# Performance work log

Measured on AMD Instinct MI355X. Metric: run time of the kernel, lower is better.

Reference implementation:

```python
import jax, jax.numpy as jnp
import numpy as np

N, E, IN_F, EDGE_F, HID, S = 200000, 600000, 28, 4, 128, 20000
NUM_LAYERS = 4
L = NUM_LAYERS - 1
BN_EPS = 1e-5


def setup_inputs() -> dict:
    key = jax.random.key(0)
    ks = jax.random.split(key, 20)
    p = lambda k, shape: (jax.random.normal(k, shape, dtype=jnp.float32) * 0.1)
    return {
        'x': jax.random.normal(ks[0], (N, IN_F), dtype=jnp.float32),
        'edge_index': jax.random.randint(ks[1], (2, E), 0, N),
        'edge_attr': jax.random.normal(ks[2], (E, EDGE_F), dtype=jnp.float32),
        'edge_weight': jax.random.uniform(ks[3], (E,), dtype=jnp.float32),
        'node_mask': (jax.random.uniform(ks[4], (N,)) > 0.5).astype(jnp.float32),
        'subgraphs2nodes': jax.random.randint(ks[5], (N,), 0, S),
        # layer-1 params (in_features -> hidden)
        'be1_W1': p(ks[6], (EDGE_F, IN_F)), 'be1_b1': jnp.zeros((IN_F,), jnp.float32),
        'be1_W2': p(ks[7], (IN_F, IN_F)), 'be1_b2': jnp.zeros((IN_F,), jnp.float32),
        'm1_W1': p(ks[8], (IN_F, HID)), 'm1_b1': jnp.zeros((HID,), jnp.float32),
        'm1_W2': p(ks[9], (HID, HID)), 'm1_b2': jnp.zeros((HID,), jnp.float32),
        'bn1_g': jnp.ones((HID,), jnp.float32), 'bn1_b': jnp.zeros((HID,), jnp.float32),
        'eps1': jnp.zeros((), jnp.float32),
        # layers 2..NUM_LAYERS, stacked (hidden -> hidden)
        'beW1': p(ks[10], (L, EDGE_F, HID)), 'beb1': jnp.zeros((L, HID), jnp.float32),
        'beW2': p(ks[11], (L, HID, HID)), 'beb2': jnp.zeros((L, HID), jnp.float32),
        'mW1': p(ks[12], (L, HID, HID)), 'mb1': jnp.zeros((L, HID), jnp.float32),
        'mW2': p(ks[13], (L, HID, HID)), 'mb2': jnp.zeros((L, HID), jnp.float32),
        'bng': jnp.ones((L, HID), jnp.float32), 'bnb': jnp.zeros((L, HID), jnp.float32),
        'eps': jnp.zeros((L,), jnp.float32),
    }


def _mlp2(h, W1, b1, W2, b2):
    # Linear -> ReLU -> Linear
    return jnp.dot(jax.nn.relu(jnp.dot(h, W1) + b1), W2) + b2


def _gine(x, src, dst, edge_attr, edge_weight, eps,
          beW1, beb1, beW2, beb2, W1, b1, W2, b2, g, beta):
    # bond encoder on edge features
    e = _mlp2(edge_attr, beW1, beb1, beW2, beb2)            # [E, d]
    # message: relu(x_j + e_ij) * w_ij, aggregated at dst via scatter-add
    m = jax.nn.relu(x[src] + e) * edge_weight[:, None]      # [E, d]
    aggr = jax.ops.segment_sum(m, dst, num_segments=N)      # [N, d]
    h = (1.0 + eps) * x + aggr
    # node MLP: Linear,ReLU,Linear,BN(train mode),ReLU
    h = _mlp2(h, W1, b1, W2, b2)
    mu = jnp.mean(h, axis=0)
    var = jnp.mean((h - mu) ** 2, axis=0)
    h = (h - mu) * jax.lax.rsqrt(var + BN_EPS) * g + beta
    return jax.nn.relu(h)


def reference(x, edge_index, edge_attr, edge_weight, node_mask, subgraphs2nodes,
              be1_W1, be1_b1, be1_W2, be1_b2, m1_W1, m1_b1, m1_W2, m1_b2,
              bn1_g, bn1_b, eps1,
              beW1, beb1, beW2, beb2, mW1, mb1, mW2, mb2, bng, bnb, eps):
    src, dst = edge_index[0], edge_index[1]
    h = _gine(x, src, dst, edge_attr, edge_weight, eps1,
              be1_W1, be1_b1, be1_W2, be1_b2,
              m1_W1, m1_b1, m1_W2, m1_b2, bn1_g, bn1_b)
    for i in range(L):
        h_new = _gine(h, src, dst, edge_attr, edge_weight, eps[i],
                      beW1[i], beb1[i], beW2[i], beb2[i],
                      mW1[i], mb1[i], mW2[i], mb2[i], bng[i], bnb[i])
        h = h + h_new  # residual
    # float node_mask branch + global_add_pool over subgraphs2nodes
    h = h * node_mask[:, None]
    return jax.ops.segment_sum(h, subgraphs2nodes, num_segments=S)  # [S, HID]
```

## Files before the change

kernel.cpp:

```cpp
#include <hip/hip_runtime.h>
#include <hip/hip_bf16.h>


#define BNEPS 1e-5f
#define LDA 136
#define SCAN_NB 240

typedef __attribute__((ext_vector_type(8))) short bf16x8;
typedef __attribute__((ext_vector_type(8))) unsigned short u16x8;
typedef __attribute__((ext_vector_type(4))) float f32x4;

__device__ inline short f2bf(float f) {
    __hip_bfloat16 h = __float2bfloat16(f);
    return *reinterpret_cast<short*>(&h);
}
__device__ inline unsigned short f2bfu(float f) {
    __hip_bfloat16 h = __float2bfloat16(f);
    return *reinterpret_cast<unsigned short*>(&h);
}
__device__ inline float bf2f(unsigned short u) {
    union { unsigned int i; float f; } v; v.i = ((unsigned int)u) << 16; return v.f;
}


__global__ __launch_bounds__(256) void k_prep(
    const float* __restrict__ m1W2, const float* __restrict__ beW2,
    const float* __restrict__ mW1, const float* __restrict__ mW2,
    short* __restrict__ out)
{
    __shared__ float tileS[64][65];
    int b = blockIdx.x, mat = b >> 2, t = b & 3;
    const float* Wsrc;
    if (mat == 0) Wsrc = m1W2;
    else {
        int l = (mat - 1) / 3, which = (mat - 1) % 3;
        Wsrc = (which == 0) ? beW2 + (size_t)l * 16384
             : (which == 1) ? mW1 + (size_t)l * 16384
             :                mW2 + (size_t)l * 16384;
    }
    short* dst = out + (size_t)mat * 16384;
    int tr = (t >> 1) * 64, tc = (t & 1) * 64;
    for (int i = threadIdx.x; i < 4096; i += 256) {
        int r = i >> 6, c = i & 63;
        tileS[r][c] = Wsrc[(size_t)(tr + r) * 128 + (tc + c)];
    }
    __syncthreads();
    for (int i = threadIdx.x; i < 4096; i += 256) {
        int kl = i & 63, nl = i >> 6;
        int n = tc + nl, k = tr + kl;
        int fo = (((n >> 4) * 4 + (k >> 5)) * 64 + (((k >> 3) & 3) * 16 + (n & 15))) * 8 + (k & 7);
        dst[fo] = f2bf(tileS[kl][nl]);
    }
}

__global__ __launch_bounds__(256) void k_prep1(
    const float* __restrict__ W1, short* __restrict__ out)
{
    for (int i = threadIdx.x; i < 4096; i += 256) {
        int j = i & 7, sub = (i >> 3) & 63, nt = i >> 9;
        int quad = sub >> 4, l15 = sub & 15;
        int n = nt * 16 + l15, k = quad * 8 + j;
        out[i] = (k < 28) ? f2bf(W1[(size_t)k * 128 + n]) : (short)0;
    }
}

__global__ __launch_bounds__(256) void k_prep28(
    const float* __restrict__ W2, short* __restrict__ out)
{
    for (int i = threadIdx.x; i < 32 * 32; i += 256) {
        int n = i >> 5, k = i & 31;
        out[i] = (n < 28 && k < 28) ? f2bf(W2[(size_t)k * 28 + n]) : (short)0;
    }
}

__global__ __launch_bounds__(256) void k_prepx(
    const float* __restrict__ x, unsigned short* __restrict__ xbf, int N)
{
    int total = N * 32;
    for (int i = blockIdx.x * 256 + threadIdx.x; i < total; i += gridDim.x * 256) {
        int n = i >> 5, c = i & 31;
        xbf[i] = (c < 28) ? f2bfu(x[(size_t)n * 28 + c]) : (unsigned short)0;
    }
}

__global__ __launch_bounds__(256) void k_count(
    const int* __restrict__ ei, int* __restrict__ counts, int E)
{
    for (int e = blockIdx.x * 256 + threadIdx.x; e < E; e += gridDim.x * 256)
        atomicAdd(&counts[ei[E + e]], 1);
}

__global__ __launch_bounds__(256) void k_count2(
    const int* __restrict__ s2n, const float* __restrict__ mask,
    int* __restrict__ counts2, int N)
{
    for (int n = blockIdx.x * 256 + threadIdx.x; n < N; n += gridDim.x * 256)
        if (mask[n] != 0.f) atomicAdd(&counts2[s2n[n]], 1);
}

__global__ __launch_bounds__(256) void k_scanA(
    const int* __restrict__ counts, int* __restrict__ bsum, int N, int seg)
{
    __shared__ int red[256];
    int b = blockIdx.x;
    int lo = b * seg, hi = min(lo + seg, N);
    int s = 0;
    for (int i = lo + threadIdx.x; i < hi; i += 256) s += counts[i];
    red[threadIdx.x] = s;
    __syncthreads();
    for (int d = 128; d > 0; d >>= 1) {
        if (threadIdx.x < d) red[threadIdx.x] += red[threadIdx.x + d];
        __syncthreads();
    }
    if (threadIdx.x == 0) bsum[b] = red[0];
}

__global__ __launch_bounds__(256) void k_scanB(
    int* __restrict__ bsum, int nb, int* __restrict__ offs, int N)
{
    __shared__ int sh[256];
    int v = (threadIdx.x < nb) ? bsum[threadIdx.x] : 0;
    sh[threadIdx.x] = v;
    __syncthreads();
    for (int d = 1; d < 256; d <<= 1) {
        int t = (threadIdx.x >= d) ? sh[threadIdx.x - d] : 0;
        __syncthreads();
        sh[threadIdx.x] += t;
        __syncthreads();
    }
    if (threadIdx.x < nb) bsum[threadIdx.x] = sh[threadIdx.x] - v;
    if (threadIdx.x == 0) offs[N] = sh[255];
}

__global__ __launch_bounds__(256) void k_scanC(
    const int* __restrict__ counts, const int* __restrict__ bsum,
    int* __restrict__ offs, int* __restrict__ cursor, int N, int seg)
{
    __shared__ int sh[256];
    int b = blockIdx.x;
    int lo = b * seg, hi = min(lo + seg, N);
    int base = bsum[b];
    for (int t0 = lo; t0 < hi; t0 += 256) {
        int i = t0 + threadIdx.x;
        int v = (i < hi) ? counts[i] : 0;
        sh[threadIdx.x] = v;
        __syncthreads();
        for (int d = 1; d < 256; d <<= 1) {
            int t = (threadIdx.x >= d) ? sh[threadIdx.x - d] : 0;
            __syncthreads();
            sh[threadIdx.x] += t;
            __syncthreads();
        }
        int excl = base + sh[threadIdx.x] - v;
        if (i < hi) { offs[i] = excl; cursor[i] = excl; }
// ... 247 lines not shown
        m += fmaxf(bf2f(xx) + bf2f(ee), 0.f) * __int_as_float(mt.y);
    GSLOT28(mtA, eA, xA, k0)
    GSLOT28(mtB, eB, xB, k0 + 1)
    GSLOT28(mtC, eC, xC, k0 + 2)
    GSLOT28(mtD, eD, xD, k0 + 3)
    int k = k0;
    while (true) {
        GCONS28(mtA, eA, xA)
        GCONS28(mtB, eB, xB)
        GCONS28(mtC, eC, xC)
        GCONS28(mtD, eD, xD)
        k += 4;
        if (k >= k1) break;
        GSLOT28(mtA, eA, xA, k)
        GSLOT28(mtB, eB, xB, k + 1)
        GSLOT28(mtC, eC, xC, k + 2)
        GSLOT28(mtD, eD, xD, k + 3)
    }
    #undef GSLOT28
    #undef GCONS28
    u28[(size_t)n * 28 + lane] = fmaf(s, x[(size_t)n * 28 + lane], m);
}

__global__ __launch_bounds__(512, 2) void k_mlp(
    const unsigned short* __restrict__ src, const short* __restrict__ W1f,
    const float* __restrict__ b1, const short* __restrict__ W2f,
    const float* __restrict__ b2, unsigned short* __restrict__ dst,
    float* __restrict__ stats, int N)
{
    __shared__ short As[256 * LDA];
    __shared__ short Bs1[16384];
    __shared__ short Bs2[16384];
    __shared__ float sstat[256];
    int tid = threadIdx.x;
    for (int i = tid; i < 2048; i += 512) {
        *(bf16x8*)&Bs1[i * 8] = *(const bf16x8*)&W1f[i * 8];
        *(bf16x8*)&Bs2[i * 8] = *(const bf16x8*)&W2f[i * 8];
    }
    if (tid < 256) sstat[tid] = 0.f;
    int w = tid >> 6, lane = tid & 63;
    int l15 = lane & 15, quad = lane >> 4;
    int rb = w * 32;
    float b1r[8], b2r[8], lsum[8], lsq[8];
    #pragma unroll
    for (int nt = 0; nt < 8; ++nt) {
        b1r[nt] = b1[nt * 16 + l15]; b2r[nt] = b2[nt * 16 + l15];
        lsum[nt] = 0.f; lsq[nt] = 0.f;
    }
    int numTiles = (N + 255) >> 8;
    bf16x8 st[8];
    {
        int tile = blockIdx.x;
        if (tile < numTiles) {
            int base = tile * 256;
            #pragma unroll
            for (int kk = 0; kk < 8; ++kk) {
                int i = tid + kk * 512;
                int rr = base + (i >> 4);
                st[kk] = (rr < N) ? *(const bf16x8*)&src[(size_t)rr * 128 + (i & 15) * 8]
                                  : (bf16x8){0, 0, 0, 0, 0, 0, 0, 0};
            }
        }
    }
    __syncthreads();

    for (int tile = blockIdx.x; tile < numTiles; tile += gridDim.x) {
        int base = tile * 256;
        #pragma unroll
        for (int kk = 0; kk < 8; ++kk) {
            int i = tid + kk * 512;
            *(bf16x8*)&As[(i >> 4) * LDA + (i & 15) * 8] = st[kk];
        }
        int tnext = tile + gridDim.x;
        if (tnext < numTiles) {
            int bn = tnext * 256;
            #pragma unroll
            for (int kk = 0; kk < 8; ++kk) {
                int i = tid + kk * 512;
                int rr = bn + (i >> 4);
                st[kk] = (rr < N) ? *(const bf16x8*)&src[(size_t)rr * 128 + (i & 15) * 8]
                                  : (bf16x8){0, 0, 0, 0, 0, 0, 0, 0};
            }
        }
        __syncthreads();
        f32x4 acc[2][8];
        #pragma unroll
        for (int rg = 0; rg < 2; ++rg)
            #pragma unroll
            for (int nt = 0; nt < 8; ++nt) acc[rg][nt] = (f32x4){0.f, 0.f, 0.f, 0.f};
        #pragma unroll
        for (int kt = 0; kt < 4; ++kt) {
            bf16x8 af0 = *(bf16x8*)&As[(rb + l15) * LDA + kt * 32 + quad * 8];
            bf16x8 af1 = *(bf16x8*)&As[(rb + 16 + l15) * LDA + kt * 32 + quad * 8];
            #pragma unroll
            for (int nt = 0; nt < 8; ++nt) {
                bf16x8 bf = *(const bf16x8*)&Bs1[((nt * 4 + kt) * 64 + lane) * 8];
                acc[0][nt] = __builtin_amdgcn_mfma_f32_16x16x32_bf16(af0, bf, acc[0][nt], 0, 0, 0);
                acc[1][nt] = __builtin_amdgcn_mfma_f32_16x16x32_bf16(af1, bf, acc[1][nt], 0, 0, 0);
            }
        }
        #pragma unroll
        for (int rg = 0; rg < 2; ++rg)
            #pragma unroll
            for (int nt = 0; nt < 8; ++nt)
                #pragma unroll
                for (int r = 0; r < 4; ++r)
                    As[(rb + rg * 16 + quad * 4 + r) * LDA + nt * 16 + l15] =
                        f2bf(fmaxf(acc[rg][nt][r] + b1r[nt], 0.f));
        #pragma unroll
        for (int rg = 0; rg < 2; ++rg)
            #pragma unroll
            for (int nt = 0; nt < 8; ++nt) acc[rg][nt] = (f32x4){0.f, 0.f, 0.f, 0.f};
        #pragma unroll
        for (int kt = 0; kt < 4; ++kt) {
            bf16x8 af0 = *(bf16x8*)&As[(rb + l15) * LDA + kt * 32 + quad * 8];
            bf16x8 af1 = *(bf16x8*)&As[(rb + 16 + l15) * LDA + kt * 32 + quad * 8];
            #pragma unroll
            for (int nt = 0; nt < 8; ++nt) {
                bf16x8 bf = *(const bf16x8*)&Bs2[((nt * 4 + kt) * 64 + lane) * 8];
                acc[0][nt] = __builtin_amdgcn_mfma_f32_16x16x32_bf16(af0, bf, acc[0][nt], 0, 0, 0);
                acc[1][nt] = __builtin_amdgcn_mfma_f32_16x16x32_bf16(af1, bf, acc[1][nt], 0, 0, 0);
            }
        }
        #pragma unroll
        for (int rg = 0; rg < 2; ++rg)
            #pragma unroll
            for (int nt = 0; nt < 8; ++nt) {
                int row0 = base + rb + rg * 16 + quad * 4;
                #pragma unroll
                for (int r = 0; r < 4; ++r) {
                    float z = acc[rg][nt][r] + b2r[nt];
                    if (row0 + r < N) { lsum[nt] += z; lsq[nt] = fmaf(z, z, lsq[nt]); }
                    As[(rb + rg * 16 + quad * 4 + r) * LDA + nt * 16 + l15] = f2bf(z);
                }
            }
        #pragma unroll
        for (int it = 0; it < 8; ++it) {
            int arow = rb + it * 4 + quad;
            int rr = base + arow;
            if (rr < N)
                *(bf16x8*)&dst[(size_t)rr * 128 + l15 * 8] = *(bf16x8*)&As[arow * LDA + l15 * 8];
        }
        __syncthreads();
    }
    #pragma unroll
    for (int nt = 0; nt < 8; ++nt) {
        atomicAdd(&sstat[nt * 16 + l15], lsum[nt]);
        atomicAdd(&sstat[128 + nt * 16 + l15], lsq[nt]);
    }
    __syncthreads();
    if (tid < 256) atomicAdd(&stats[tid], sstat[tid]);
}

__global__ __launch_bounds__(512, 2) void k_mlp1(
    const float* __restrict__ u28, const short* __restrict__ W1f,
    const float* __restrict__ b1, const short* __restrict__ W2f,
    const float* __restrict__ b2, unsigned short* __restrict__ dst,
    float* __restrict__ stats, int N)
{
    __shared__ short A28[256 * 40];
    __shared__ short As[256 * LDA];
    __shared__ short Bs1[4096];
    __shared__ short Bs2[16384];
    __shared__ float sstat[256];
    int tid = threadIdx.x;
    if (tid < 512) {
        int i = tid;
        *(bf16x8*)&Bs1[i * 8] = *(const bf16x8*)&W1f[i * 8];
    }
    for (int i = tid; i < 2048; i += 512)
        *(bf16x8*)&Bs2[i * 8] = *(const bf16x8*)&W2f[i * 8];
    for (int i = tid; i < 1024; i += 512) {
        int row = i >> 2, c = 28 + (i & 3);
        A28[row * 40 + c] = 0;
    }
    if (tid < 256) sstat[tid] = 0.f;
    int w = tid >> 6, lane = tid & 63;
    int l15 = lane & 15, quad = lane >> 4;
    int rb = w * 32;
    float b1r[8], b2r[8], lsum[8], lsq[8];
    #pragma unroll
    for (int nt = 0; nt < 8; ++nt) {
        b1r[nt] = b1[nt * 16 + l15]; b2r[nt] = b2[nt * 16 + l15];
        lsum[nt] = 0.f; lsq[nt] = 0.f;
    }
    int numTiles = (N + 255) >> 8;
    float stf[14];
    {
        int tile = blockIdx.x;
        if (tile < numTiles) {
            int base = tile * 256;
            #pragma unroll
            for (int kk = 0; kk < 14; ++kk) {
                int idx = tid + kk * 512;
                int row = idx / 28, col = idx - row * 28;
                int rr = base + row;
                stf[kk] = (rr < N) ? u28[(size_t)rr * 28 + col] : 0.f;
            }
        }
    }
    __syncthreads();

    for (int tile = blockIdx.x; tile < numTiles; tile += gridDim.x) {
        int base = tile * 256;
        #pragma unroll
        for (int kk = 0; kk < 14; ++kk) {
            int idx = tid + kk * 512;
            int row = idx / 28, col = idx - row * 28;
            A28[row * 40 + col] = f2bf(stf[kk]);
        }
        int tnext = tile + gridDim.x;
        if (tnext < numTiles) {
            int bn = tnext * 256;
            #pragma unroll
            for (int kk = 0; kk < 14; ++kk) {
                int idx = tid + kk * 512;
                int row = idx / 28, col = idx - row * 28;
                int rr = bn + row;
                stf[kk] = (rr < N) ? u28[(size_t)rr * 28 + col] : 0.f;
            }
        }
        __syncthreads();
        f32x4 acc[2][8];
        #pragma unroll
        for (int rg = 0; rg < 2; ++rg)
            #pragma unroll
            for (int nt = 0; nt < 8; ++nt) acc[rg][nt] = (f32x4){0.f, 0.f, 0.f, 0.f};
        {
            bf16x8 af0 = *(bf16x8*)&A28[(rb + l15) * 40 + quad * 8];
            bf16x8 af1 = *(bf16x8*)&A28[(rb + 16 + l15) * 40 + quad * 8];
            #pragma unroll
            for (int nt = 0; nt < 8; ++nt) {
                bf16x8 bf = *(const bf16x8*)&Bs1[(nt * 64 + lane) * 8];
                acc[0][nt] = __builtin_amdgcn_mfma_f32_16x16x32_bf16(af0, bf, acc[0][nt], 0, 0, 0);
                acc[1][nt] = __builtin_amdgcn_mfma_f32_16x16x32_bf16(af1, bf, acc[1][nt], 0, 0, 0);
            }
        }
        #pragma unroll
        for (int rg = 0; rg < 2; ++rg)
            #pragma unroll
            for (int nt = 0; nt < 8; ++nt)
                #pragma unroll
                for (int r = 0; r < 4; ++r)
                    As[(rb + rg * 16 + quad * 4 + r) * LDA + nt * 16 + l15] =
                        f2bf(fmaxf(acc[rg][nt][r] + b1r[nt], 0.f));
        __syncthreads();
        #pragma unroll
        for (int rg = 0; rg < 2; ++rg)
            #pragma unroll
            for (int nt = 0; nt < 8; ++nt) acc[rg][nt] = (f32x4){0.f, 0.f, 0.f, 0.f};
        #pragma unroll
        for (int kt = 0; kt < 4; ++kt) {
            bf16x8 af0 = *(bf16x8*)&As[(rb + l15) * LDA + kt * 32 + quad * 8];
            bf16x8 af1 = *(bf16x8*)&As[(rb + 16 + l15) * LDA + kt * 32 + quad * 8];
            #pragma unroll
            for (int nt = 0; nt < 8; ++nt) {
                bf16x8 bf = *(const bf16x8*)&Bs2[((nt * 4 + kt) * 64 + lane) * 8];
                acc[0][nt] = __builtin_amdgcn_mfma_f32_16x16x32_bf16(af0, bf, acc[0][nt], 0, 0, 0);
                acc[1][nt] = __builtin_amdgcn_mfma_f32_16x16x32_bf16(af1, bf, acc[1][nt], 0, 0, 0);
            }
        }
        #pragma unroll
        for (int rg = 0; rg < 2; ++rg)
            #pragma unroll
            for (int nt = 0; nt < 8; ++nt) {
                int row0 = base + rb + rg * 16 + quad * 4;
                #pragma unroll
                for (int r = 0; r < 4; ++r) {
                    float z = acc[rg][nt][r] + b2r[nt];
                    if (row0 + r < N) { lsum[nt] += z; lsq[nt] = fmaf(z, z, lsq[nt]); }
                    As[(rb + rg * 16 + quad * 4 + r) * LDA + nt * 16 + l15] = f2bf(z);
                }
            }
        #pragma unroll
        for (int it = 0; it < 8; ++it) {
            int arow = rb + it * 4 + quad;
            int rr = base + arow;
            if (rr < N)
                *(bf16x8*)&dst[(size_t)rr * 128 + l15 * 8] = *(bf16x8*)&As[arow * LDA + l15 * 8];
        }
        __syncthreads();
    }
    #pragma unroll
    for (int nt = 0; nt < 8; ++nt) {
        atomicAdd(&sstat[nt * 16 + l15], lsum[nt]);
        atomicAdd(&sstat[128 + nt * 16 + l15], lsq[nt]);
    }
    __syncthreads();
    if (tid < 256) atomicAdd(&stats[tid], sstat[tid]);
}

__global__ __launch_bounds__(256) void k_bn(
    const unsigned short* __restrict__ z, const float* __restrict__ stats,
    const float* __restrict__ g, const float* __restrict__ bb, float invN,
    unsigned short* __restrict__ h, int residual, int N)
{
    __shared__ float ss[256];
    if (threadIdx.x < 128) {
        int j = threadIdx.x;
        float mu  = stats[j] * invN;
        float var = fmaf(stats[128 + j], invN, -mu * mu);
        float sc  = rsqrtf(fmaxf(var, 0.f) + BNEPS) * g[j];
        ss[j] = sc;
        ss[128 + j] = fmaf(-mu, sc, bb[j]);
    }
    __syncthreads();
    int idx8 = blockIdx.x * 256 + threadIdx.x;
    int stride = gridDim.x * 256;
    int c0 = (idx8 & 15) * 8;
    float scl[8], sht[8];
    #pragma unroll
    for (int r = 0; r < 8; ++r) { scl[r] = ss[c0 + r]; sht[r] = ss[128 + c0 + r]; }
    int total8 = N * 16;
    for (; idx8 < total8; idx8 += stride) {
        int n = idx8 >> 4;
        u16x8 z8 = *(const u16x8*)&z[(size_t)n * 128 + c0];
        float hn[8];
        #pragma unroll
        for (int r = 0; r < 8; ++r)
            hn[r] = fmaxf(fmaf(bf2f(z8[r]), scl[r], sht[r]), 0.f);
        if (residual) {
            u16x8 h8 = *(const u16x8*)&h[(size_t)n * 128 + c0];
            #pragma unroll
            for (int r = 0; r < 8; ++r) hn[r] += bf2f(h8[r]);
        }
        u16x8 o;
        #pragma unroll
        for (int r = 0; r < 8; ++r) o[r] = f2bfu(hn[r]);
        *(u16x8*)&h[(size_t)n * 128 + c0] = o;
    }
}

__global__ __launch_bounds__(256) void k_poolbn(
    const unsigned short* __restrict__ z, const unsigned short* __restrict__ hprev,
    const float* __restrict__ stats, const float* __restrict__ g,
    const float* __restrict__ bb, float invN,
    const int* __restrict__ offs2, const int* __restrict__ perm2,
    float* __restrict__ out, int S)
{
    __shared__ float ss[256];
    if (threadIdx.x < 128) {
        int j = threadIdx.x;
        float mu  = stats[j] * invN;
        float var = fmaf(stats[128 + j], invN, -mu * mu);
        float sc  = rsqrtf(fmaxf(var, 0.f) + BNEPS) * g[j];
        ss[j] = sc;
        ss[128 + j] = fmaf(-mu, sc, bb[j]);
    }
    __syncthreads();
    int w = threadIdx.x >> 6, lane = threadIdx.x & 63;
    int s = blockIdx.x * 4 + w;
    if (s >= S) return;
    int c0 = lane * 2;
    float scl0 = ss[c0], scl1 = ss[c0 + 1];
    float sht0 = ss[128 + c0], sht1 = ss[128 + c0 + 1];
    int k0 = offs2[s], k1 = offs2[s + 1];
    float a0 = 0.f, a1 = 0.f;
    for (int k = k0; k < k1; ++k) {
        int n = perm2[k];
        ushort2 zv = *(const ushort2*)&z[(size_t)n * 128 + c0];
        ushort2 hv = *(const ushort2*)&hprev[(size_t)n * 128 + c0];
        a0 += fmaxf(fmaf(bf2f(zv.x), scl0, sht0), 0.f) + bf2f(hv.x);
        a1 += fmaxf(fmaf(bf2f(zv.y), scl1, sht1), 0.f) + bf2f(hv.y);
    }
    *(float2*)&out[(size_t)s * 128 + c0] = make_float2(a0, a1);
}

extern "C" void kernel_launch(void* const* d_in, const int* in_sizes, int n_in,
                              void* d_out, int out_size, void* d_ws, size_t ws_size,
                              hipStream_t stream) {
    const float* x    = (const float*)d_in[0];
    const int*   ei   = (const int*)d_in[1];
    const float* ea   = (const float*)d_in[2];
    const float* ew   = (const float*)d_in[3];
    const float* mask = (const float*)d_in[4];
    const int*   s2n  = (const int*)d_in[5];
    const float* be1W1 = (const float*)d_in[6];
    const float* be1b1 = (const float*)d_in[7];
    const float* be1W2 = (const float*)d_in[8];
    const float* be1b2 = (const float*)d_in[9];
    const float* m1W1  = (const float*)d_in[10];
    const float* m1b1  = (const float*)d_in[11];
    const float* m1W2  = (const float*)d_in[12];
    const float* m1b2  = (const float*)d_in[13];
    const float* bn1g  = (const float*)d_in[14];
    const float* bn1b  = (const float*)d_in[15];
    const float* eps1  = (const float*)d_in[16];
    const float* beW1  = (const float*)d_in[17];
    const float* beb1  = (const float*)d_in[18];
    const float* beW2  = (const float*)d_in[19];
    const float* beb2  = (const float*)d_in[20];
    const float* mW1   = (const float*)d_in[21];
    const float* mb1   = (const float*)d_in[22];
    const float* mW2   = (const float*)d_in[23];
    const float* mb2   = (const float*)d_in[24];
    const float* bng   = (const float*)d_in[25];
    const float* bnb   = (const float*)d_in[26];
    const float* epsL  = (const float*)d_in[27];

    const int N = in_sizes[0] / 28;
    const int E = in_sizes[1] / 2;
    const int S = out_size / 128;
    const float invN = 1.0f / (float)N;
    const int NS = N / 2;
    const int EMC = E / 2 + 8192;

    auto al16 = [](size_t v) { return (v + 15) & ~(size_t)15; };
    char* ws = (char*)d_ws;
    size_t offH      = 0;
    size_t offA0     = al16(offH + (size_t)N * 256);
    size_t offEm     = al16(offA0 + (size_t)N * 256);
    size_t emBytes   = (size_t)EMC * 256;
    if ((size_t)E * 56 > emBytes) emBytes = (size_t)E * 56;
    size_t offStats  = al16(offEm + emBytes);
    size_t offSS     = al16(offStats + 4096);
    size_t offWts    = al16(offSS + 1024);
    size_t offCounts = al16(offWts + 10 * 16384 * 2 + 4096 * 2 + 1024 * 2);
    size_t offOffs   = al16(offCounts + (size_t)N * 4);
    size_t offCursor = al16(offOffs + (size_t)(N + 1) * 4);
    size_t offPmeta  = al16(offCursor + (size_t)N * 4);
    size_t offPea    = al16(offPmeta + (size_t)E * 8);
    size_t offBsum   = al16(offPea + (size_t)E * 16);
    size_t offCnt2   = al16(offBsum + SCAN_NB * 4);
    size_t offOffs2  = al16(offCnt2 + (size_t)S * 4);
    size_t offCur2   = al16(offOffs2 + (size_t)(S + 1) * 4);
    size_t offPerm2  = al16(offCur2 + (size_t)S * 4);
    size_t need      = offPerm2 + (size_t)N * 4;
    if (ws_size < need) return;

    unsigned short* h    = (unsigned short*)(ws + offH);
    unsigned short* a0   = (unsigned short*)(ws + offA0);
    unsigned short* emsg = (unsigned short*)(ws + offEm);
    float* u28    = (float*)(ws + offA0);
    unsigned short* xbf = (unsigned short*)(ws + offA0 + 26214400);
    float* stats  = (float*)(ws + offStats);
    short* wts    = (short*)(ws + offWts);
    short* w1p    = wts + 10 * 16384;
    short* w2p28  = w1p + 4096;
    int*   counts = (int*)(ws + offCounts);
    int*   offs   = (int*)(ws + offOffs);
    int*   cursor = (int*)(ws + offCursor);
    int2*  pmeta  = (int2*)(ws + offPmeta);
    float4* pea4  = (float4*)(ws + offPea);
    int*   bsum   = (int*)(ws + offBsum);
    int*   cnt2   = (int*)(ws + offCnt2);
    int*   offs2  = (int*)(ws + offOffs2);
    int*   cur2   = (int*)(ws + offCur2);
    int*   perm2  = (int*)(ws + offPerm2);
    const float4* ea4 = (const float4*)ea;

    hipMemsetAsync(stats, 0, 4 * 256 * sizeof(float), stream);
    hipMemsetAsync(counts, 0, (size_t)N * sizeof(int), stream);
    hipMemsetAsync(cnt2, 0, (size_t)S * sizeof(int), stream);

    k_prep<<<40, 256, 0, stream>>>(m1W2, beW2, mW1, mW2, wts);
    k_prep1<<<1, 256, 0, stream>>>(m1W1, w1p);
    k_prep28<<<1, 256, 0, stream>>>(be1W2, w2p28);
    k_prepx<<<512, 256, 0, stream>>>(x, xbf, N);

    const int seg = (N + SCAN_NB - 1) / SCAN_NB;
    k_count<<<1024, 256, 0, stream>>>(ei, counts, E);
    k_scanA<<<SCAN_NB, 256, 0, stream>>>(counts, bsum, N, seg);
    k_scanB<<<1, 256, 0, stream>>>(bsum, SCAN_NB, offs, N);
    k_scanC<<<SCAN_NB, 256, 0, stream>>>(counts, bsum, offs, cursor, N, seg);
    k_scatter<<<1024, 256, 0, stream>>>(ei, ew, ea4, cursor, pmeta, pea4, E);

    const int seg2 = (S + SCAN_NB - 1) / SCAN_NB;
    k_count2<<<512, 256, 0, stream>>>(s2n, mask, cnt2, N);
    k_scanA<<<SCAN_NB, 256, 0, stream>>>(cnt2, bsum, S, seg2);
    k_scanB<<<1, 256, 0, stream>>>(bsum, SCAN_NB, offs2, S);
    k_scanC<<<SCAN_NB, 256, 0, stream>>>(cnt2, bsum, offs2, cur2, S, seg2);
    k_scatter2<<<512, 256, 0, stream>>>(s2n, mask, cur2, perm2, N);

    auto wt_be = [&](int l) { return wts + (size_t)(1 + 3 * l + 0) * 16384; };
    auto wt_m1 = [&](int l) { return wts + (size_t)(1 + 3 * l + 1) * 16384; };
    auto wt_m2 = [&](int l) { return wts + (size_t)(1 + 3 * l + 2) * 16384; };

    k_emsg28_mm<<<2048, 256, 0, stream>>>(pea4, be1W1, be1b1, w2p28, be1b2, emsg, E);
    k_gather28<<<(N + 7) / 8, 256, 0, stream>>>(x, xbf, offs, pmeta, emsg, eps1, u28, N);
    k_mlp1<<<256, 512, 0, stream>>>(u28, w1p, m1b1, wts , m1b2, h, stats, N);
    k_bn<<<2048, 256, 0, stream>>>(h, stats, bn1g, bn1b, invN, h, 0, N);

    for (int l = 0; l < 3; ++l) {
        for (int c = 0; c < 2; ++c) {
            int n0 = (c == 0) ? 0 : NS;
            int n1 = (c == 0) ? NS : N;
            k_emsg<<<2048, 256, 0, stream>>>(pea4,
                beW1 + (size_t)l * 512, beb1 + (size_t)l * 128,
                wt_be(l), beb2 + (size_t)l * 128, emsg, offs, n0, n1);
            k_gather<<<(n1 - n0 + 7) / 8, 256, 0, stream>>>(h, offs, pmeta, emsg, a0,
                epsL, l, n0, n1);
        }
        k_mlp<<<256, 512, 0, stream>>>(a0, wt_m1(l), mb1 + (size_t)l * 128,
                                       wt_m2(l), mb2 + (size_t)l * 128, a0,
                                       stats + 256 * (l + 1), N);
        if (l < 2) {
            k_bn<<<2048, 256, 0, stream>>>(a0, stats + 256 * (l + 1),
                bng + (size_t)l * 128, bnb + (size_t)l * 128, invN, h, 1, N);
        }
    }

    k_poolbn<<<(S + 3) / 4, 256, 0, stream>>>(a0, h, stats + 256 * 3,
        bng + 256, bnb + 256, invN, offs2, perm2, (float*)d_out, S);
}
```

Measured before the change: 1.003 ms.

## Fuse node MLP and BatchNorm apply via cooperative grid sync with register-held outputs

Replaces the separate node-MLP kernel and BatchNorm kernel with a cooperative kernel. Each block computes its tiles (fixed four per block over 256 blocks), keeps the bf16 pre-BN outputs packed in registers, does a grid-wide sync after accumulating the statistics, then applies BN, ReLU and the residual and writes h. This removes the round trip of the intermediate z through global memory and one kernel launch per layer. In exchange it adds heavy register pressure (128 extra registers per thread), a grid barrier, and it drops the previous load prefetching. It also hard-codes four tiles per block, so correctness depends on N ≤ 256*1024.

```diff
diff --git a/kernel.cpp b/kernel.cpp
--- a/kernel.cpp
+++ b/kernel.cpp
@@ -1,5 +1,8 @@
 #include <hip/hip_runtime.h>
 #include <hip/hip_bf16.h>
+#include <hip/hip_cooperative_groups.h>
+
+namespace cg = cooperative_groups;
 
 
 #define BNEPS 1e-5f
@@ -553,11 +556,174 @@
     if (tid < 256) atomicAdd(&stats[tid], sstat[tid]);
 }
 
-__global__ __launch_bounds__(512, 2) void k_mlp1(
+__global__ __launch_bounds__(512, 2) void k_mlpbn(
+    const unsigned short* __restrict__ src, const short* __restrict__ W1f,
+    const float* __restrict__ b1, const short* __restrict__ W2f,
+    const float* __restrict__ b2, unsigned short* __restrict__ hbuf,
+    float* __restrict__ stats, const float* __restrict__ g,
+    const float* __restrict__ bb, float invN, int N)
+{
+    __shared__ short As[256 * LDA];
+    __shared__ short Bs1[16384];
+    __shared__ short Bs2[16384];
+    __shared__ float sstat[256];
+    int tid = threadIdx.x;
+    for (int i = tid; i < 2048; i += 512) {
+        *(bf16x8*)&Bs1[i * 8] = *(const bf16x8*)&W1f[i * 8];
+        *(bf16x8*)&Bs2[i * 8] = *(const bf16x8*)&W2f[i * 8];
+    }
+    if (tid < 256) sstat[tid] = 0.f;
+    int w = tid >> 6, lane = tid & 63;
+    int l15 = lane & 15, quad = lane >> 4;
+    int rb = w * 32;
+    float b1r[8], b2r[8], lsum[8], lsq[8];
+    #pragma unroll
+    for (int nt = 0; nt < 8; ++nt) {
+        b1r[nt] = b1[nt * 16 + l15]; b2r[nt] = b2[nt * 16 + l15];
+        lsum[nt] = 0.f; lsq[nt] = 0.f;
+    }
+    unsigned int zreg[4][32];
+    int numTiles = (N + 255) >> 8;
+    __syncthreads();
+
+    #pragma unroll
+    for (int ti = 0; ti < 4; ++ti) {
+        int tile = (int)blockIdx.x + ti * 256;
+        if (tile < numTiles) {
+            int base = tile * 256;
+            #pragma unroll
+            for (int kk = 0; kk < 8; ++kk) {
+                int i = tid + kk * 512;
+                int rr = base + (i >> 4);
+                bf16x8 v = (rr < N) ? *(const bf16x8*)&src[(size_t)rr * 128 + (i & 15) * 8]
+                                    : (bf16x8){0, 0, 0, 0, 0, 0, 0, 0};
+                *(bf16x8*)&As[(i >> 4) * LDA + (i & 15) * 8] = v;
+            }
+            __syncthreads();
+            f32x4 acc[2][8];
+            #pragma unroll
+            for (int rg = 0; rg < 2; ++rg)
+                #pragma unroll
+                for (int nt = 0; nt < 8; ++nt) acc[rg][nt] = (f32x4){0.f, 0.f, 0.f, 0.f};
+            #pragma unroll
+            for (int kt = 0; kt < 4; ++kt) {
+                bf16x8 af0 = *(bf16x8*)&As[(rb + l15) * LDA + kt * 32 + quad * 8];
+                bf16x8 af1 = *(bf16x8*)&As[(rb + 16 + l15) * LDA + kt * 32 + quad * 8];
+                #pragma unroll
+                for (int nt = 0; nt < 8; ++nt) {
+                    bf16x8 bf = *(const bf16x8*)&Bs1[((nt * 4 + kt) * 64 + lane) * 8];
+                    acc[0][nt] = __builtin_amdgcn_mfma_f32_16x16x32_bf16(af0, bf, acc[0][nt], 0, 0, 0);
+                    acc[1][nt] = __builtin_amdgcn_mfma_f32_16x16x32_bf16(af1, bf, acc[1][nt], 0, 0, 0);
+                }
+            }
+            #pragma unroll
+            for (int rg = 0; rg < 2; ++rg)
+                #pragma unroll
+                for (int nt = 0; nt < 8; ++nt)
+                    #pragma unroll
+                    for (int r = 0; r < 4; ++r)
+                        As[(rb + rg * 16 + quad * 4 + r) * LDA + nt * 16 + l15] =
+                            f2bf(fmaxf(acc[rg][nt][r] + b1r[nt], 0.f));
+            #pragma unroll
+            for (int rg = 0; rg < 2; ++rg)
+                #pragma unroll
+                for (int nt = 0; nt < 8; ++nt) acc[rg][nt] = (f32x4){0.f, 0.f, 0.f, 0.f};
+            #pragma unroll
+            for (int kt = 0; kt < 4; ++kt) {
+                bf16x8 af0 = *(bf16x8*)&As[(rb + l15) * LDA + kt * 32 + quad * 8];
+                bf16x8 af1 = *(bf16x8*)&As[(rb + 16 + l15) * LDA + kt * 32 + quad * 8];
+                #pragma unroll
+                for (int nt = 0; nt < 8; ++nt) {
+                    bf16x8 bf = *(const bf16x8*)&Bs2[((nt * 4 + kt) * 64 + lane) * 8];
+                    acc[0][nt] = __builtin_amdgcn_mfma_f32_16x16x32_bf16(af0, bf, acc[0][nt], 0, 0, 0);
+                    acc[1][nt] = __builtin_amdgcn_mfma_f32_16x16x32_bf16(af1, bf, acc[1][nt], 0, 0, 0);
+                }
+            }
+            #pragma unroll
+            for (int rg = 0; rg < 2; ++rg)
+                #pragma unroll
+                for (int nt = 0; nt < 8; ++nt) {
+                    int row0 = base + rb + rg * 16 + quad * 4;
+                    float zv0 = acc[rg][nt][0] + b2r[nt];
+                    float zv1 = acc[rg][nt][1] + b2r[nt];
+                    float zv2 = acc[rg][nt][2] + b2r[nt];
+                    float zv3 = acc[rg][nt][3] + b2r[nt];
+                    if (row0 + 0 < N) { lsum[nt] += zv0; lsq[nt] = fmaf(zv0, zv0, lsq[nt]); }
+                    if (row0 + 1 < N) { lsum[nt] += zv1; lsq[nt] = fmaf(zv1, zv1, lsq[nt]); }
+                    if (row0 + 2 < N) { lsum[nt] += zv2; lsq[nt] = fmaf(zv2, zv2, lsq[nt]); }
+                    if (row0 + 3 < N) { lsum[nt] += zv3; lsq[nt] = fmaf(zv3, zv3, lsq[nt]); }
+                    zreg[ti][rg * 16 + nt * 2 + 0] = ((unsigned int)f2bfu(zv1) << 16) | f2bfu(zv0);
+                    zreg[ti][rg * 16 + nt * 2 + 1] = ((unsigned int)f2bfu(zv3) << 16) | f2bfu(zv2);
+                }
+            __syncthreads();
+        }
+    }
+    #pragma unroll
+    for (int nt = 0; nt < 8; ++nt) {
+        atomicAdd(&sstat[nt * 16 + l15], lsum[nt]);
+        atomicAdd(&sstat[128 + nt * 16 + l15], lsq[nt]);
+    }
+    __syncthreads();
+    if (tid < 256) atomicAdd(&stats[tid], sstat[tid]);
+    __threadfence();
+    cg::this_grid().sync();
+    if (tid < 128) {
+        const volatile float* vs = stats;
+        float mu  = vs[tid] * invN;
+        float var = fmaf(vs[128 + tid], invN, -mu * mu);
+        float sc  = rsqrtf(fmaxf(var, 0.f) + BNEPS) * g[tid];
+        sstat[tid] = sc;
+        sstat[128 + tid] = fmaf(-mu, sc, bb[tid]);
+    }
+    __syncthreads();
+    float scl[8], sht[8];
+    #pragma unroll
+    for (int nt = 0; nt < 8; ++nt) {
+        int col = nt * 16 + l15;
+        scl[nt] = sstat[col]; sht[nt] = sstat[128 + col];
+    }
+    #pragma unroll
+    for (int ti = 0; ti < 4; ++ti) {
+        int tile = (int)blockIdx.x + ti * 256;
+        if (tile < numTiles) {
+            int base = tile * 256;
+            #pragma unroll
+            for (int rg = 0; rg < 2; ++rg)
+                #pragma unroll
+                for (int nt = 0; nt < 8; ++nt)
+                    #pragma unroll
+                    for (int p = 0; p < 2; ++p) {
+                        unsigned int pk = zreg[ti][rg * 16 + nt * 2 + p];
+                        float y0 = fmaxf(fmaf(bf2f((unsigned short)(pk & 0xffff)), scl[nt], sht[nt]), 0.f);
+                        float y1 = fmaxf(fmaf(bf2f((unsigned short)(pk >> 16)), scl[nt], sht[nt]), 0.f);
+                        int row = rb + rg * 16 + quad * 4 + p * 2;
+                        As[row * LDA + nt * 16 + l15] = f2bf(y0);
+                        As[(row + 1) * LDA + nt * 16 + l15] = f2bf(y1);
+                    }
+            #pragma unroll
+            for (int it = 0; it < 8; ++it) {
+                int arow = rb + it * 4 + quad;
+                int rr = base + arow;
+                if (rr < N) {
+                    u16x8 yv = *(u16x8*)&As[arow * LDA + l15 * 8];
+                    u16x8 hv = *(const u16x8*)&hbuf[(size_t)rr * 128 + l15 * 8];
+                    u16x8 o;
+                    #pragma unroll
+                    for (int r = 0; r < 8; ++r)
+                        o[r] = f2bfu(bf2f(yv[r]) + bf2f(hv[r]));
+                    *(u16x8*)&hbuf[(size_t)rr * 128 + l15 * 8] = o;
+                }
+            }
+        }
+    }
+}
+
+__global__ __launch_bounds__(512, 2) void k_mlpbn1(
     const float* __restrict__ u28, const short* __restrict__ W1f,
     const float* __restrict__ b1, const short* __restrict__ W2f,
-    const float* __restrict__ b2, unsigned short* __restrict__ dst,
-    float* __restrict__ stats, int N)
+    const float* __restrict__ b2, unsigned short* __restrict__ hbuf,
+    float* __restrict__ stats, const float* __restrict__ g,
+    const float* __restrict__ bb, float invN, int N)
 {
     __shared__ short A28[256 * 40];
     __shared__ short As[256 * LDA];
@@ -565,10 +731,8 @@
     __shared__ short Bs2[16384];
     __shared__ float sstat[256];
     int tid = threadIdx.x;
-    if (tid < 512) {
-        int i = tid;
-        *(bf16x8*)&Bs1[i * 8] = *(const bf16x8*)&W1f[i * 8];
-    }
+    if (tid < 512)
+        *(bf16x8*)&Bs1[tid * 8] = *(const bf16x8*)&W1f[tid * 8];
     for (int i = tid; i < 2048; i += 512)
         *(bf16x8*)&Bs2[i * 8] = *(const bf16x8*)&W2f[i * 8];
     for (int i = tid; i < 1024; i += 512) {
@@ -585,102 +749,77 @@
         b1r[nt] = b1[nt * 16 + l15]; b2r[nt] = b2[nt * 16 + l15];
         lsum[nt] = 0.f; lsq[nt] = 0.f;
     }
+    unsigned int zreg[4][32];
     int numTiles = (N + 255) >> 8;
-    float stf[14];
-    {
-        int tile = blockIdx.x;
+    __syncthreads();
+
+    #pragma unroll
+    for (int ti = 0; ti < 4; ++ti) {
+        int tile = (int)blockIdx.x + ti * 256;
         if (tile < numTiles) {
             int base = tile * 256;
-            #pragma unroll
-            for (int kk = 0; kk < 14; ++kk) {
-                int idx = tid + kk * 512;
-                int row = idx / 28, col = idx - row * 28;
+            for (int i = tid; i < 256 * 28; i += 512) {
+                int row = i / 28, col = i - row * 28;
                 int rr = base + row;
-                stf[kk] = (rr < N) ? u28[(size_t)rr * 28 + col] : 0.f;
-            }
-        }
-    }
-    __syncthreads();
-
-    for (int tile = blockIdx.x; tile < numTiles; tile += gridDim.x) {
-        int base = tile * 256;
-        #pragma unroll
-        for (int kk = 0; kk < 14; ++kk) {
-            int idx = tid + kk * 512;
-            int row = idx / 28, col = idx - row * 28;
-            A28[row * 40 + col] = f2bf(stf[kk]);
-        }
-        int tnext = tile + gridDim.x;
-        if (tnext < numTiles) {
-            int bn = tnext * 256;
-            #pragma unroll
-            for (int kk = 0; kk < 14; ++kk) {
-                int idx = tid + kk * 512;
-                int row = idx / 28, col = idx - row * 28;
-                int rr = bn + row;
-                stf[kk] = (rr < N) ? u28[(size_t)rr * 28 + col] : 0.f;
-            }
-        }
-        __syncthreads();
-        f32x4 acc[2][8];
-        #pragma unroll
-        for (int rg = 0; rg < 2; ++rg)
-            #pragma unroll
-            for (int nt = 0; nt < 8; ++nt) acc[rg][nt] = (f32x4){0.f, 0.f, 0.f, 0.f};
-        {
-            bf16x8 af0 = *(bf16x8*)&A28[(rb + l15) * 40 + quad * 8];
-            bf16x8 af1 = *(bf16x8*)&A28[(rb + 16 + l15) * 40 + quad * 8];
-            #pragma unroll
-            for (int nt = 0; nt < 8; ++nt) {
-                bf16x8 bf = *(const bf16x8*)&Bs1[(nt * 64 + lane) * 8];
-                acc[0][nt] = __builtin_amdgcn_mfma_f32_16x16x32_bf16(af0, bf, acc[0][nt], 0, 0, 0);
-                acc[1][nt] = __builtin_amdgcn_mfma_f32_16x16x32_bf16(af1, bf, acc[1][nt], 0, 0, 0);
-            }
-        }
-        #pragma unroll
-        for (int rg = 0; rg < 2; ++rg)
-            #pragma unroll
-            for (int nt = 0; nt < 8; ++nt)
-                #pragma unroll
-                for (int r = 0; r < 4; ++r)
-                    As[(rb + rg * 16 + quad * 4 + r) * LDA + nt * 16 + l15] =
-                        f2bf(fmaxf(acc[rg][nt][r] + b1r[nt], 0.f));
-        __syncthreads();
-        #pragma unroll
-        for (int rg = 0; rg < 2; ++rg)
-            #pragma unroll
-            for (int nt = 0; nt < 8; ++nt) acc[rg][nt] = (f32x4){0.f, 0.f, 0.f, 0.f};
-        #pragma unroll
-        for (int kt = 0; kt < 4; ++kt) {
-            bf16x8 af0 = *(bf16x8*)&As[(rb + l15) * LDA + kt * 32 + quad * 8];
-            bf16x8 af1 = *(bf16x8*)&As[(rb + 16 + l15) * LDA + kt * 32 + quad * 8];
-            #pragma unroll
-            for (int nt = 0; nt < 8; ++nt) {
-                bf16x8 bf = *(const bf16x8*)&Bs2[((nt * 4 + kt) * 64 + lane) * 8];
-                acc[0][nt] = __builtin_amdgcn_mfma_f32_16x16x32_bf16(af0, bf, acc[0][nt], 0, 0, 0);
-                acc[1][nt] = __builtin_amdgcn_mfma_f32_16x16x32_bf16(af1, bf, acc[1][nt], 0, 0, 0);
-            }
-        }
-        #pragma unroll
-        for (int rg = 0; rg < 2; ++rg)
-            #pragma unroll
-            for (int nt = 0; nt < 8; ++nt) {
-                int row0 = base + rb + rg * 16 + quad * 4;
-                #pragma unroll
-                for (int r = 0; r < 4; ++r) {
-                    float z = acc[rg][nt][r] + b2r[nt];
-                    if (row0 + r < N) { lsum[nt] += z; lsq[nt] = fmaf(z, z, lsq[nt]); }
-                    As[(rb + rg * 16 + quad * 4 + r) * LDA + nt * 16 + l15] = f2bf(z);
+                A28[row * 40 + col] = (rr < N) ? f2bf(u28[(size_t)rr * 28 + col]) : (short)0;
+            }
+            __syncthreads();
+            f32x4 acc[2][8];
+            #pragma unroll
+            for (int rg = 0; rg < 2; ++rg)
+                #pragma unroll
+                for (int nt = 0; nt < 8; ++nt) acc[rg][nt] = (f32x4){0.f, 0.f, 0.f, 0.f};
+            {
+                bf16x8 af0 = *(bf16x8*)&A28[(rb + l15) * 40 + quad * 8];
+                bf16x8 af1 = *(bf16x8*)&A28[(rb + 16 + l15) * 40 + quad * 8];
+                #pragma unroll
+                for (int nt = 0; nt < 8; ++nt) {
+                    bf16x8 bf = *(const bf16x8*)&Bs1[(nt * 64 + lane) * 8];
+                    acc[0][nt] = __builtin_amdgcn_mfma_f32_16x16x32_bf16(af0, bf, acc[0][nt], 0, 0, 0);
+                    acc[1][nt] = __builtin_amdgcn_mfma_f32_16x16x32_bf16(af1, bf, acc[1][nt], 0, 0, 0);
                 }
             }
-        #pragma unroll
-        for (int it = 0; it < 8; ++it) {
-            int arow = rb + it * 4 + quad;
-            int rr = base + arow;
-            if (rr < N)
-                *(bf16x8*)&dst[(size_t)rr * 128 + l15 * 8] = *(bf16x8*)&As[arow * LDA + l15 * 8];
-        }
-        __syncthreads();
+            #pragma unroll
+            for (int rg = 0; rg < 2; ++rg)
+                #pragma unroll
+                for (int nt = 0; nt < 8; ++nt)
+                    #pragma unroll
+                    for (int r = 0; r < 4; ++r)
+                        As[(rb + rg * 16 + quad * 4 + r) * LDA + nt * 16 + l15] =
+                            f2bf(fmaxf(acc[rg][nt][r] + b1r[nt], 0.f));
+            #pragma unroll
+            for (int rg = 0; rg < 2; ++rg)
+                #pragma unroll
+                for (int nt = 0; nt < 8; ++nt) acc[rg][nt] = (f32x4){0.f, 0.f, 0.f, 0.f};
+            #pragma unroll
+            for (int kt = 0; kt < 4; ++kt) {
+                bf16x8 af0 = *(bf16x8*)&As[(rb + l15) * LDA + kt * 32 + quad * 8];
+                bf16x8 af1 = *(bf16x8*)&As[(rb + 16 + l15) * LDA + kt * 32 + quad * 8];
+                #pragma unroll
+                for (int nt = 0; nt < 8; ++nt) {
+                    bf16x8 bf = *(const bf16x8*)&Bs2[((nt * 4 + kt) * 64 + lane) * 8];
+                    acc[0][nt] = __builtin_amdgcn_mfma_f32_16x16x32_bf16(af0, bf, acc[0][nt], 0, 0, 0);
+                    acc[1][nt] = __builtin_amdgcn_mfma_f32_16x16x32_bf16(af1, bf, acc[1][nt], 0, 0, 0);
+                }
+            }
+            #pragma unroll
+            for (int rg = 0; rg < 2; ++rg)
+                #pragma unroll
+                for (int nt = 0; nt < 8; ++nt) {
+                    int row0 = base + rb + rg * 16 + quad * 4;
+                    float zv0 = acc[rg][nt][0] + b2r[nt];
+                    float zv1 = acc[rg][nt][1] + b2r[nt];
+                    float zv2 = acc[rg][nt][2] + b2r[nt];
+                    float zv3 = acc[rg][nt][3] + b2r[nt];
+                    if (row0 + 0 < N) { lsum[nt] += zv0; lsq[nt] = fmaf(zv0, zv0, lsq[nt]); }
+                    if (row0 + 1 < N) { lsum[nt] += zv1; lsq[nt] = fmaf(zv1, zv1, lsq[nt]); }
+                    if (row0 + 2 < N) { lsum[nt] += zv2; lsq[nt] = fmaf(zv2, zv2, lsq[nt]); }
+                    if (row0 + 3 < N) { lsum[nt] += zv3; lsq[nt] = fmaf(zv3, zv3, lsq[nt]); }
+                    zreg[ti][rg * 16 + nt * 2 + 0] = ((unsigned int)f2bfu(zv1) << 16) | f2bfu(zv0);
+                    zreg[ti][rg * 16 + nt * 2 + 1] = ((unsigned int)f2bfu(zv3) << 16) | f2bfu(zv2);
+                }
+            __syncthreads();
+        }
     }
     #pragma unroll
     for (int nt = 0; nt < 8; ++nt) {
@@ -689,46 +828,49 @@
     }
     __syncthreads();
     if (tid < 256) atomicAdd(&stats[tid], sstat[tid]);
-}
-
-__global__ __launch_bounds__(256) void k_bn(
-    const unsigned short* __restrict__ z, const float* __restrict__ stats,
-    const float* __restrict__ g, const float* __restrict__ bb, float invN,
-    unsigned short* __restrict__ h, int residual, int N)
-{
-    __shared__ float ss[256];
-    if (threadIdx.x < 128) {
-        int j = threadIdx.x;
-        float mu  = stats[j] * invN;
-        float var = fmaf(stats[128 + j], invN, -mu * mu);
-        float sc  = rsqrtf(fmaxf(var, 0.f) + BNEPS) * g[j];
-        ss[j] = sc;
-        ss[128 + j] = fmaf(-mu, sc, bb[j]);
-    }
-    __syncthreads();
-    int idx8 = blockIdx.x * 256 + threadIdx.x;
-    int stride = gridDim.x * 256;
-    int c0 = (idx8 & 15) * 8;
+    __threadfence();
+    cg::this_grid().sync();
+    if (tid < 128) {
+        const volatile float* vs = stats;
+        float mu  = vs[tid] * invN;
+        float var = fmaf(vs[128 + tid], invN, -mu * mu);
+        float sc  = rsqrtf(fmaxf(var, 0.f) + BNEPS) * g[tid];
+        sstat[tid] = sc;
+        sstat[128 + tid] = fmaf(-mu, sc, bb[tid]);
+    }
+    __syncthreads();
     float scl[8], sht[8];
     #pragma unroll
-    for (int r = 0; r < 8; ++r) { scl[r] = ss[c0 + r]; sht[r] = ss[128 + c0 + r]; }
-    int total8 = N * 16;
-    for (; idx8 < total8; idx8 += stride) {
-        int n = idx8 >> 4;
-        u16x8 z8 = *(const u16x8*)&z[(size_t)n * 128 + c0];
-        float hn[8];
-        #pragma unroll
-        for (int r = 0; r < 8; ++r)
-            hn[r] = fmaxf(fmaf(bf2f(z8[r]), scl[r], sht[r]), 0.f);
-        if (residual) {
-            u16x8 h8 = *(const u16x8*)&h[(size_t)n * 128 + c0];
-            #pragma unroll
-            for (int r = 0; r < 8; ++r) hn[r] += bf2f(h8[r]);
-        }
-        u16x8 o;
-        #pragma unroll
-        for (int r = 0; r < 8; ++r) o[r] = f2bfu(hn[r]);
-        *(u16x8*)&h[(size_t)n * 128 + c0] = o;
+    for (int nt = 0; nt < 8; ++nt) {
+        int col = nt * 16 + l15;
+        scl[nt] = sstat[col]; sht[nt] = sstat[128 + col];
+    }
+    #pragma unroll
+    for (int ti = 0; ti < 4; ++ti) {
+        int tile = (int)blockIdx.x + ti * 256;
+        if (tile < numTiles) {
+            int base = tile * 256;
+            #pragma unroll
+            for (int rg = 0; rg < 2; ++rg)
+                #pragma unroll
+                for (int nt = 0; nt < 8; ++nt)
+                    #pragma unroll
+                    for (int p = 0; p < 2; ++p) {
+                        unsigned int pk = zreg[ti][rg * 16 + nt * 2 + p];
+                        float y0 = fmaxf(fmaf(bf2f((unsigned short)(pk & 0xffff)), scl[nt], sht[nt]), 0.f);
+                        float y1 = fmaxf(fmaf(bf2f((unsigned short)(pk >> 16)), scl[nt], sht[nt]), 0.f);
+                        int row = rb + rg * 16 + quad * 4 + p * 2;
+                        As[row * LDA + nt * 16 + l15] = f2bf(y0);
+                        As[(row + 1) * LDA + nt * 16 + l15] = f2bf(y1);
+                    }
+            #pragma unroll
+            for (int it = 0; it < 8; ++it) {
+                int arow = rb + it * 4 + quad;
+                int rr = base + arow;
+                if (rr < N)
+                    *(u16x8*)&hbuf[(size_t)rr * 128 + l15 * 8] = *(u16x8*)&As[arow * LDA + l15 * 8];
+            }
+        }
     }
 }
 
@@ -879,8 +1021,24 @@
 
     k_emsg28_mm<<<2048, 256, 0, stream>>>(pea4, be1W1, be1b1, w2p28, be1b2, emsg, E);
     k_gather28<<<(N + 7) / 8, 256, 0, stream>>>(x, xbf, offs, pmeta, emsg, eps1, u28, N);
-    k_mlp1<<<256, 512, 0, stream>>>(u28, w1p, m1b1, wts , m1b2, h, stats, N);
-    k_bn<<<2048, 256, 0, stream>>>(h, stats, bn1g, bn1b, invN, h, 0, N);
+    {
+        const float* u28c = u28;
+        const short* w1fc = w1p;
+        const float* b1c = m1b1;
+        const short* w2fc = wts;
+        const float* b2c = m1b2;
+        unsigned short* hc = h;
+        float* stc = stats;
+        const float* gc = bn1g;
+        const float* bbc = bn1b;
+        float invNc = invN;
+        int Nc = N;
+        void* args[] = { (void*)&u28c, (void*)&w1fc, (void*)&b1c, (void*)&w2fc,
+                         (void*)&b2c, (void*)&hc, (void*)&stc, (void*)&gc,
+                         (void*)&bbc, (void*)&invNc, (void*)&Nc };
+        hipLaunchCooperativeKernel((const void*)k_mlpbn1, dim3(256), dim3(512),
+                                   args, 0, stream);
+    }
 
     for (int l = 0; l < 3; ++l) {
         for (int c = 0; c < 2; ++c) {
@@ -892,12 +1050,27 @@
             k_gather<<<(n1 - n0 + 7) / 8, 256, 0, stream>>>(h, offs, pmeta, emsg, a0,
                 epsL, l, n0, n1);
         }
-        k_mlp<<<256, 512, 0, stream>>>(a0, wt_m1(l), mb1 + (size_t)l * 128,
-                                       wt_m2(l), mb2 + (size_t)l * 128, a0,
-                                       stats + 256 * (l + 1), N);
         if (l < 2) {
-            k_bn<<<2048, 256, 0, stream>>>(a0, stats + 256 * (l + 1),
-                bng + (size_t)l * 128, bnb + (size_t)l * 128, invN, h, 1, N);
+            const unsigned short* srcc = a0;
+            const short* w1fc = wt_m1(l);
+            const float* b1c = mb1 + (size_t)l * 128;
+            const short* w2fc = wt_m2(l);
+            const float* b2c = mb2 + (size_t)l * 128;
+            unsigned short* hc = h;
+            float* stc = stats + 256 * (l + 1);
+            const float* gc = bng + (size_t)l * 128;
+            const float* bbc = bnb + (size_t)l * 128;
+            float invNc = invN;
+            int Nc = N;
+            void* args[] = { (void*)&srcc, (void*)&w1fc, (void*)&b1c, (void*)&w2fc,
+                             (void*)&b2c, (void*)&hc, (void*)&stc, (void*)&gc,
+                             (void*)&bbc, (void*)&invNc, (void*)&Nc };
+            hipLaunchCooperativeKernel((const void*)k_mlpbn, dim3(256), dim3(512),
+                                       args, 0, stream);
+        } else {
+            k_mlp<<<256, 512, 0, stream>>>(a0, wt_m1(l), mb1 + (size_t)l * 128,
+                                           wt_m2(l), mb2 + (size_t)l * 128, a0,
+                                           stats + 256 * (l + 1), N);
         }
     }
 
```

New measurement: 1.291 ms. +28.8%, slower.
